# Performance work log

Measured on AMD Instinct MI355X. Metric: run time of the kernel, lower is better.

The kernel has to match this reference:

```python
import jax, jax.numpy as jnp
import numpy as np
from math import sqrt

D, H, B, L = 1024, 16, 2, 2048
DK = D // H

def linear(x, w, b):
    # torch Linear layout: w (out, in)
    return x @ w.T + b

def conv1d(x, w, b, padding, groups=1):
    # x: (B, C, L); w: (O, I/groups, K) -> torch Conv1d semantics
    y = jax.lax.conv_general_dilated(
        x, w, window_strides=(1,), padding=(padding,),
        dimension_numbers=('NCH', 'OIH', 'NCH'), feature_group_count=groups)
    return y + b[None, :, None]

def setup_inputs() -> dict:
    key = jax.random.key(0)
    ks = jax.random.split(key, 26)
    def n(k, shape, s=0.02):
        return jax.random.normal(k, shape, jnp.float32) * s
    return {
        'x': jax.random.normal(ks[0], (B, L, D), jnp.float32),
        'Wq_w': n(ks[1], (D, D)), 'Wq_b': n(ks[2], (D,)),
        'Wk_w': n(ks[3], (D, D)), 'Wk_b': n(ks[4], (D,)),
        'Wv_w': n(ks[5], (D, D)), 'Wv_b': n(ks[6], (D,)),
        'convq_w': n(ks[7], (D, D, 3)), 'convq_b': n(ks[8], (D,)),
        'convk_w': n(ks[9], (D, D, 3)), 'convk_b': n(ks[10], (D,)),
        'qproj_w': n(ks[11], (D, 2 * D)), 'qproj_b': n(ks[12], (D,)),
        'kproj_w': n(ks[13], (D, 2 * D)), 'kproj_b': n(ks[14], (D,)),
        'tau1_w': n(ks[15], (2 * D, 1, 3)), 'tau1_b': n(ks[16], (2 * D,)),
        'tau2_w': n(ks[17], (H, 2 * D, 1)), 'tau2_b': n(ks[18], (H,)),
        'del1_w': n(ks[19], (2 * D, 1, 3)), 'del1_b': n(ks[20], (2 * D,)),
        'del2_w': n(ks[21], (H, 2 * D, 1)), 'del2_b': n(ks[22], (H,)),
        'out_w': n(ks[23], (D, D)), 'out_b': n(ks[24], (D,)),
    }

def reference(x, Wq_w, Wq_b, Wk_w, Wk_b, Wv_w, Wv_b,
              convq_w, convq_b, convk_w, convk_b,
              qproj_w, qproj_b, kproj_w, kproj_b,
              tau1_w, tau1_b, tau2_w, tau2_b,
              del1_w, del1_b, del2_w, del2_b,
              out_w, out_b):
    b_, l_, _ = x.shape

    # Q branch: linear -> conv3 -> concat -> proj
    q_in = linear(x, Wq_w, Wq_b).transpose(0, 2, 1)          # (B, D, L)
    Q3 = conv1d(q_in, convq_w, convq_b, (1, 1))              # (B, D, L)
    Q_cat = jnp.concatenate([q_in, Q3], axis=1).transpose(0, 2, 1)  # (B, L, 2D)
    Q = linear(Q_cat, qproj_w, qproj_b).reshape(b_, l_, H, DK).transpose(0, 2, 1, 3)

    # K branch
    k_in = linear(x, Wk_w, Wk_b).transpose(0, 2, 1)
    K3 = conv1d(k_in, convk_w, convk_b, (1, 1))
    K_cat = jnp.concatenate([k_in, K3], axis=1).transpose(0, 2, 1)
    K = linear(K_cat, kproj_w, kproj_b).reshape(b_, l_, H, DK).transpose(0, 2, 1, 3)

    V = linear(x, Wv_w, Wv_b).reshape(b_, l_, H, DK).transpose(0, 2, 1, 3)

    # per-head tau (query-row scale) and delta (key-column bias), shape (B, H, L)
    x_conv = x.transpose(0, 2, 1)                             # (B, D, L)
    tau = jax.nn.sigmoid(conv1d(
        jax.nn.gelu(conv1d(x_conv, tau1_w, tau1_b, (1, 1), groups=D), approximate=False),
        tau2_w, tau2_b, (0, 0)))
    delta = jax.nn.sigmoid(conv1d(
        jax.nn.gelu(conv1d(x_conv, del1_w, del1_b, (1, 1), groups=D), approximate=False),
        del2_w, del2_b, (0, 0)))

    scores = jnp.einsum('bhqd,bhkd->bhqk', Q, K) / sqrt(DK)   # (B, H, L, L)
    scores = scores * tau[..., None] + delta[:, :, None, :]
    attn = jax.nn.softmax(scores, axis=-1)                    # dropout = identity (eval)
    out = jnp.einsum('bhqk,bhkd->bhqd', attn, V)
    out = out.transpose(0, 2, 1, 3).reshape(b_, l_, D)
    return linear(out, out_w, out_b)
```

## Files before the change

### kernel.cpp

```cpp
#include <hip/hip_runtime.h>

typedef __bf16 bf16_t;
typedef __bf16 bf16x8 __attribute__((ext_vector_type(8)));
typedef __bf16 bf16x4 __attribute__((ext_vector_type(4)));
typedef float f32x4 __attribute__((ext_vector_type(4)));

__device__ __forceinline__ void gload_lds16(const bf16_t* g, bf16_t* l) {
  __builtin_amdgcn_global_load_lds(
      (__attribute__((address_space(1))) void*)g,
      (__attribute__((address_space(3))) void*)l, 16, 0, 0);
}

__global__ void k_detect(const unsigned int* __restrict__ xw, int* __restrict__ flag) {
  __shared__ int red[256];
  int c = 0;
  for (int j = 0; j < 16; ++j) {
    unsigned int w = xw[threadIdx.x + (j << 8)];
    unsigned int e = (w >> 7) & 0xFF;
    c += (e >= 100 && e <= 150) ? 1 : 0;
  }
  red[threadIdx.x] = c;
  __syncthreads();
  for (int s = 128; s > 0; s >>= 1) {
    if (threadIdx.x < s) red[threadIdx.x] += red[threadIdx.x + s];
    __syncthreads();
  }
  if (threadIdx.x == 0) flag[0] = (red[0] > 2048) ? 1 : 0;
}

__device__ __constant__ long c_offs[26] = {
    0, 4194304, 4195328, 4196352, 4197376, 4198400, 4199424, 6296576,
    6297600, 8394752, 8395776, 8401920, 8403968, 8436736, 8436752,
    8442896, 8444944, 8477712, 8477728,
    0, 1048576, 2097152, 3145728,
    0, 1048576, 1049600};
struct CanonArgs { const void* src[18]; };

__global__ void k_canon(CanonArgs a, int base, int n, const int* __restrict__ flag,
                        bf16_t* __restrict__ dst) {
  long e0 = ((long)blockIdx.x * 256 + threadIdx.x) * 8;
  if (e0 >= c_offs[base + n]) return;
  int k = 0;
  while (e0 >= c_offs[base + k + 1]) ++k;
  const long rel = e0 - c_offs[base + k];
  if (flag[0]) {
    *(bf16x8*)&dst[e0] = *(const bf16x8*)((const bf16_t*)a.src[k] + rel);
  } else {
    const float* sf = (const float*)a.src[k] + rel;
    f32x4 lo = *(const f32x4*)sf;
    f32x4 hi = *(const f32x4*)(sf + 4);
    bf16x8 o;
    o[0] = (bf16_t)lo[0]; o[1] = (bf16_t)lo[1]; o[2] = (bf16_t)lo[2]; o[3] = (bf16_t)lo[3];
    o[4] = (bf16_t)hi[0]; o[5] = (bf16_t)hi[1]; o[6] = (bf16_t)hi[2]; o[7] = (bf16_t)hi[3];
    *(bf16x8*)&dst[e0] = o;
  }
}

__global__ void k_zero_pads(bf16_t* __restrict__ pad, bf16_t* __restrict__ zvec) {
  int idx = blockIdx.x * 256 + threadIdx.x;
  if (idx < 1024) zvec[idx] = (bf16_t)0.0f;
  if (idx >= 8192) return;
  int b = idx >> 11;
  int r = (idx >> 10) & 1;
  int c = idx & 1023;
  long row = (long)b * 2050 + (r ? 2049 : 0);
  pad[row * 1024 + c] = (bf16_t)0.0f;
}

__global__ __launch_bounds__(256) void k_ctT(
    const void* __restrict__ wq, const void* __restrict__ wk,
    bf16_t* __restrict__ dq, bf16_t* __restrict__ dk,
    const int* __restrict__ flag) {
  __shared__ bf16_t T[64][72];
  int blk = blockIdx.x;
  const int br = blk >= 768;
  if (br) blk -= 768;
  const void* w = br ? wk : wq;
  bf16_t* dst = br ? dk : dq;
  const int ot = blk / 48, jt = blk - ot * 48;
  const int o0 = ot << 6, j0 = jt << 6;
  const int t = threadIdx.x;
  const int f = flag[0];
#pragma unroll
  for (int it = 0; it < 2; ++it) {
    const int ch = t + (it << 8);
    const int r = ch >> 3, c8 = (ch & 7) << 3;
    const long off = (long)(o0 + r) * 3072 + j0 + c8;
    if (f) {
      *(bf16x8*)&T[r][c8] = *(const bf16x8*)((const bf16_t*)w + off);
    } else {
      const float* sf = (const float*)w + off;
      bf16x8 o8;
#pragma unroll
      for (int e = 0; e < 8; ++e) o8[e] = (bf16_t)sf[e];
      *(bf16x8*)&T[r][c8] = o8;
    }
  }
  __syncthreads();
  const int j = t >> 2, oc0 = (t & 3) << 4;
  const int jj = j0 + j;
  const int drow = (jj % 3) * 1024 + jj / 3;
  bf16_t* dp = dst + (long)drow * 1024 + o0 + oc0;
#pragma unroll
  for (int s = 0; s < 16; ++s) dp[s] = T[oc0 + s][j];
}

__global__ void k_addwp1(bf16_t* __restrict__ Hq, bf16_t* __restrict__ Hk,
                         const bf16_t* __restrict__ qp, const bf16_t* __restrict__ kp) {
  const long e0 = ((long)blockIdx.x * 256 + threadIdx.x) * 8;
  if (e0 >= 2097152L) return;
  const int br = (int)(e0 >> 20);
  const int rem = (int)(e0 & 1048575);
  const int o = rem >> 10, i = rem & 1023;
  bf16_t* h = (br ? Hk : Hq) + (long)o * 3072 + 1024 + i;
  const bf16_t* w = (br ? kp : qp) + (long)o * 2048 + i;
  bf16x8 a = *(const bf16x8*)h;
  bf16x8 b = *(const bf16x8*)w;
  bf16x8 r;
#pragma unroll
  for (int e = 0; e < 8; ++e) r[e] = (bf16_t)((float)a[e] + (float)b[e]);
  *(bf16x8*)h = r;
}

__global__ __launch_bounds__(256) void k_bvec(
    const bf16_t* __restrict__ qp, const bf16_t* __restrict__ kp,
    const bf16_t* __restrict__ cqb, const bf16_t* __restrict__ ckb,
    const bf16_t* __restrict__ qpb, const bf16_t* __restrict__ kpb,
    bf16_t* __restrict__ bvec) {
  const int idx = blockIdx.x * 256 + threadIdx.x;
  if (idx >= 2048) return;
  const int br = idx >> 10, o = idx & 1023;
  const bf16_t* wrow = (br ? kp : qp) + (long)o * 2048 + 1024;
  const bf16_t* cb = br ? ckb : cqb;
  float s = 0.f;
  for (int m8 = 0; m8 < 1024; m8 += 8) {
    bf16x8 w8 = *(const bf16x8*)&wrow[m8];
    bf16x8 c8 = *(const bf16x8*)&cb[m8];
#pragma unroll
    for (int e = 0; e < 8; ++e) s += (float)w8[e] * (float)c8[e];
  }
  bvec[idx] = (bf16_t)(s + (float)((br ? kpb : qpb)[o]));
}

struct GemmP {
  const bf16_t *A0;
  const bf16_t *B0, *B1, *B2;
  const bf16_t *bias0, *bias1, *bias2;
  bf16_t *C0, *C1, *C2;
  long a_jump, at_jump;
  long cj0, cj1, cj2, ct_jump;
  long b_jump;
  int rpb, rpt, lda, ldb, bsel_by_n, bshift, K, csel_by_n;
  int crs0, ccs0, crs1, ccs1, crs2, ccs2;
};

template <int BN, bool FINAL>
__global__ __launch_bounds__(256) void k_gemm(GemmP p, const int* __restrict__ flagp) {
  __shared__ __align__(16) bf16_t As[2][4096];
  __shared__ __align__(16) bf16_t Bs[2][BN * 32];
  const int tid = threadIdx.x;
  const int gx = gridDim.x;
  int lin = blockIdx.y * gx + blockIdx.x;
  const int nwg = gx * gridDim.y;
  lin = ((lin & 7) * (nwg >> 3)) + (lin >> 3);
  const int n0 = (lin % gx) * BN;
  const int m0 = (lin / gx) << 7;
  const int batch = m0 / p.rpb;
  const int tap = (m0 - batch * p.rpb) / p.rpt;
  const int bidx = p.bsel_by_n ? (n0 >> 10) : (m0 >> p.bshift);
  const bf16_t* Bp = p.b_jump ? (p.B0 + (long)bidx * p.b_jump)
                              : (bidx == 0 ? p.B0 : (bidx == 1 ? p.B1 : p.B2));
  const bf16_t* biasp = bidx == 0 ? p.bias0 : (bidx == 1 ? p.bias1 : p.bias2);
  const long abase = (long)batch * p.a_jump + (long)tap * p.at_jump;
  const int arow = tid >> 2;
  const int koff = (((tid & 3) ^ ((tid >> 3) & 3)) << 3);
  const int wid = tid >> 6, lane = tid & 63;
  const int l15 = lane & 15, lg = lane >> 4;
  const int nloc = n0 & 1023;

  constexpr int MI = (BN == 128) ? 4 : 2;
  const int wr = (BN == 128) ? ((wid >> 1) << 6) : (wid << 5);
  const int wc = (BN == 128) ? ((wid & 1) << 6) : 0;
  const int rsw = ((lg ^ (l15 >> 1)) & 3) << 3;

  f32x4 acc[MI][4];
#pragma unroll
  for (int i = 0; i < MI; ++i)
#pragma unroll
    for (int j = 0; j < 4; ++j) acc[i][j] = (f32x4){0.f, 0.f, 0.f, 0.f};

  auto stage = [&](int bufi, int k) {
    const int kg = k + koff;
#pragma unroll
    for (int half = 0; half < 2; ++half) {
      const int row = m0 + half * 64 + arow;
      gload_lds16(p.A0 + abase + (long)row * p.lda + kg,
                  &As[bufi][half * 2048 + (tid << 3)]);
    }
    gload_lds16(Bp + (long)(nloc + arow) * p.ldb + kg, &Bs[bufi][tid << 3]);
    if (BN == 128)
      gload_lds16(Bp + (long)(nloc + 64 + arow) * p.ldb + kg, &Bs[bufi][2048 + (tid << 3)]);
  };

  const int nk = p.K >> 5;
  int buf = 0;
  stage(0, 0);
  asm volatile("s_waitcnt vmcnt(0)" ::: "memory");
  __builtin_amdgcn_s_barrier();
  __builtin_amdgcn_sched_barrier(0);
  for (int kt = 0; kt < nk; ++kt) {
    if (kt + 1 < nk) stage(buf ^ 1, (kt + 1) << 5);
    bf16x8 af[MI], bfr[4];
#pragma unroll
    for (int i = 0; i < MI; ++i)
      af[i] = *(const bf16x8*)&As[buf][((wr + (i << 4) + l15) << 5) + rsw];
#pragma unroll
    for (int j = 0; j < 4; ++j)
      bfr[j] = *(const bf16x8*)&Bs[buf][((wc + (j << 4) + l15) << 5) + rsw];
#pragma unroll
    for (int i = 0; i < MI; ++i)
#pragma unroll
      for (int j = 0; j < 4; ++j)
        acc[i][j] = __builtin_amdgcn_mfma_f32_16x16x32_bf16(af[i], bfr[j], acc[i][j], 0, 0, 0);
    if (kt + 1 < nk) asm volatile("s_waitcnt vmcnt(0)" ::: "memory");
    __builtin_amdgcn_s_barrier();
    __builtin_amdgcn_sched_barrier(0);
    buf ^= 1;
  }

  const int cp = p.csel_by_n ? (n0 >> 10) : (m0 >> p.bshift);
  bf16_t* Cb = cp == 0 ? p.C0 : (cp == 1 ? p.C1 : p.C2);
  const int crs = cp == 0 ? p.crs0 : (cp == 1 ? p.crs1 : p.crs2);
  const int ccs = cp == 0 ? p.ccs0 : (cp == 1 ? p.ccs1 : p.ccs2);
  const long cj = cp == 0 ? p.cj0 : (cp == 1 ? p.cj1 : p.cj2);
  const bool f32out = FINAL && (flagp[0] == 0);
  const long cbase = (long)batch * cj + (long)tap * p.ct_jump;
#pragma unroll
  for (int i = 0; i < MI; ++i) {
    const int row = m0 + wr + (i << 4) + (lg << 2);
#pragma unroll
    for (int j = 0; j < 4; ++j) {
      const int col = nloc + wc + (j << 4) + l15;
      const float bv = (float)biasp[col];
#pragma unroll
      for (int r = 0; r < 4; ++r) {
        const float val = acc[i][j][r] + bv;
        const long ci = cbase + (long)(row + r) * crs + (long)col * ccs;
        if (FINAL && f32out) ((float*)Cb)[ci] = val;
        else Cb[ci] = (bf16_t)val;
      }
    }
  }
}

__global__ __launch_bounds__(256) void k_taudelta(
    const bf16_t* __restrict__ x,
    const bf16_t* __restrict__ t1w, const bf16_t* __restrict__ t1b,
    const bf16_t* __restrict__ t2w, const bf16_t* __restrict__ t2b,
    const bf16_t* __restrict__ d1w, const bf16_t* __restrict__ d1b,
    const bf16_t* __restrict__ d2w, const bf16_t* __restrict__ d2b,
    float* __restrict__ tau, float* __restrict__ dlt)
{
  const int bt = blockIdx.x;
  const int t = bt & 2047;
  const int b = bt >> 11;
  const int tid = threadIdx.x;
  const bf16_t* xr = x + ((long)bt << 10);

  float acc[32];
#pragma unroll
  for (int i = 0; i < 32; ++i) acc[i] = 0.f;

  for (int j = 0; j < 8; ++j) {
    const int c = tid + (j << 8);
    const int src = c >> 1;
    const float x0 = (float)xr[src];
    const float xm = (t > 0) ? (float)xr[src - 1024] : 0.f;
    const float xp = (t < 2047) ? (float)xr[src + 1024] : 0.f;
    float st = (float)t1w[3 * c] * xm + (float)t1w[3 * c + 1] * x0 +
               (float)t1w[3 * c + 2] * xp + (float)t1b[c];
    float sd = (float)d1w[3 * c] * xm + (float)d1w[3 * c + 1] * x0 +
               (float)d1w[3 * c + 2] * xp + (float)d1b[c];
    const float gt = 0.5f * st * (1.f + erff(st * 0.70710678118f));
    const float gd = 0.5f * sd * (1.f + erff(sd * 0.70710678118f));
#pragma unroll
    for (int h = 0; h < 16; ++h) {
      acc[h]      += (float)t2w[(h << 11) + c] * gt;
      acc[16 + h] += (float)d2w[(h << 11) + c] * gd;
    }
  }

  __shared__ float red[256][33];
  __shared__ float red2[8][32];
#pragma unroll
  for (int i = 0; i < 32; ++i) red[tid][i] = acc[i];
  __syncthreads();
  const int i = tid & 31, g = tid >> 5;
  float p = 0.f;
#pragma unroll
  for (int k2 = 0; k2 < 32; ++k2) p += red[(g << 5) + k2][i];
  __syncthreads();
  red2[g][i] = p;
  __syncthreads();
  if (tid < 32) {
    float s = 0.f;
#pragma unroll
    for (int g2 = 0; g2 < 8; ++g2) s += red2[g2][tid];
    const int h = tid & 15;
    if (tid < 16) {
      s += (float)t2b[h];
      tau[((long)((b << 4) + h) << 11) + t] = 1.f / (1.f + __expf(-s));
    } else {
      s += (float)d2b[h];
      dlt[((long)((b << 4) + h) << 11) + t] =
          1.4426950408889634f / (1.f + __expf(-s));
    }
  }
}

__device__ __forceinline__ unsigned pk2(float a, float b) {
  union { bf16_t h[2]; unsigned u; } z;
  z.h[0] = (bf16_t)a; z.h[1] = (bf16_t)b;
  return z.u;
}

__global__ __launch_bounds__(256) void k_attn(
    const bf16_t* __restrict__ QKb, const bf16_t* __restrict__ VT,
    const float* __restrict__ tau, const float* __restrict__ dlt,
    bf16_t* __restrict__ O)
{
  const int lin = blockIdx.x;
  const int wg = ((lin & 7) << 7) + (lin >> 3);
  const int bh = wg >> 5, qt = wg & 31;
  const int tid = threadIdx.x;
  const int lane = tid & 63;
  const int wid = tid >> 6;
  const int l15 = lane & 15, lg = lane >> 4;
  const int b = bh >> 4, h = bh & 15;
  const int qbase = (qt << 6) + (wid << 4);

  const bf16_t* Qp = QKb + ((long)b << 21) + (h << 6);
  const bf16_t* Kp = QKb + 4194304 + ((long)b << 21) + (h << 6);
  const bf16_t* Vp = VT + ((long)bh << 17);
  const float* dltb = dlt + ((long)bh << 11);

  __shared__ __align__(16) bf16_t Ks[2][4096];
  __shared__ __align__(16) bf16_t Vs[2][4096];
  __shared__ unsigned Plds[4][16][32];

  bf16x8 qf[2];
#pragma unroll
  for (int kd = 0; kd < 2; ++kd)
    qf[kd] = *(const bf16x8*)&Qp[((long)(qbase + l15) << 10) + (kd << 5) + (lg << 3)];
  const float tq = tau[((long)bh << 11) + qbase + l15] * (0.125f * 1.4426950408889634f);

  bf16x8 onesf;
#pragma unroll
  for (int e = 0; e < 8; ++e) onesf[e] = (bf16_t)1.0f;

  f32x4 accO[4];
#pragma unroll
  for (int d = 0; d < 4; ++d) accO[d] = (f32x4){0.f, 0.f, 0.f, 0.f};
  f32x4 accL = (f32x4){0.f, 0.f, 0.f, 0.f};

  const int xr = (l15 & 7) << 2;

  auto stageKV = [&](int bufi, int kk) {
#pragma unroll
    for (int it = 0; it < 2; ++it) {
      const int t2 = tid + (it << 8);
      const int r = t2 >> 3, cc = (t2 & 7) ^ (r & 7);
      gload_lds16(Kp + ((long)(kk + r) << 10) + (cc << 3), &Ks[bufi][t2 << 3]);
    }
#pragma unroll
    for (int it = 0; it < 2; ++it) {
      const int t2 = tid + (it << 8);
      const int r = t2 >> 3;
      gload_lds16(Vp + ((long)r << 11) + kk + (((t2 & 7) ^ (r & 7)) << 3), &Vs[bufi][t2 << 3]);
    }
  };

  int buf = 0;
  stageKV(0, 0);
  asm volatile("s_waitcnt vmcnt(0)" ::: "memory");
  __builtin_amdgcn_s_barrier();
  __builtin_amdgcn_sched_barrier(0);

  for (int kk = 0; kk < 2048; kk += 64) {
    if (kk + 64 < 2048) stageKV(buf ^ 1, kk + 64);

    f32x4 st[4];
    __builtin_amdgcn_s_setprio(1);
#pragma unroll
    for (int kb = 0; kb < 4; ++kb) {
      f32x4 z = (f32x4){0.f, 0.f, 0.f, 0.f};
#pragma unroll
      for (int kd = 0; kd < 2; ++kd) {
        const bf16x8 kf = *(const bf16x8*)&Ks[buf][(((kb << 4) + l15) << 6) +
                                                  ((((kd << 2) | lg) ^ (l15 & 7)) << 3)];
        z = __builtin_amdgcn_mfma_f32_16x16x32_bf16(kf, qf[kd], z, 0, 0, 0);
      }
      st[kb] = z;
    }
    __builtin_amdgcn_s_setprio(0);

#pragma unroll
    for (int kb = 0; kb < 4; ++kb) {
      const f32x4 dl = *(const f32x4*)&dltb[kk + (kb << 4) + (lg << 2)];
      const float p0 = exp2f(fminf(fmaf(st[kb][0], tq, dl[0]), 30.f));
      const float p1 = exp2f(fminf(fmaf(st[kb][1], tq, dl[1]), 30.f));
      const float p2 = exp2f(fminf(fmaf(st[kb][2], tq, dl[2]), 30.f));
      const float p3 = exp2f(fminf(fmaf(st[kb][3], tq, dl[3]), 30.f));
      Plds[wid][l15][((kb << 3) + (lg << 1)) ^ xr]       = pk2(p0, p1);
      Plds[wid][l15][(((kb << 3) + (lg << 1)) | 1) ^ xr] = pk2(p2, p3);
    }
    asm volatile("s_waitcnt lgkmcnt(0)" ::: "memory");
    __builtin_amdgcn_sched_barrier(0);
    const bf16x8 pf0 = *(const bf16x8*)&Plds[wid][l15][(lg << 2) ^ xr];
    const bf16x8 pf1 = *(const bf16x8*)&Plds[wid][l15][(16 | (lg << 2)) ^ xr];
    asm volatile("s_waitcnt lgkmcnt(0)" ::: "memory");
    __builtin_amdgcn_sched_barrier(0);

    __builtin_amdgcn_s_setprio(1);
#pragma unroll
    for (int d = 0; d < 4; ++d) {
      const bf16x8 vf0 = *(const bf16x8*)&Vs[buf][(((d << 4) + l15) << 6) +
                                                 ((lg ^ (l15 & 7)) << 3)];
      const bf16x8 vf1 = *(const bf16x8*)&Vs[buf][(((d << 4) + l15) << 6) +
                                                 (((4 | lg) ^ (l15 & 7)) << 3)];
      accO[d] = __builtin_amdgcn_mfma_f32_16x16x32_bf16(vf0, pf0, accO[d], 0, 0, 0);
      accO[d] = __builtin_amdgcn_mfma_f32_16x16x32_bf16(vf1, pf1, accO[d], 0, 0, 0);
    }
    accL = __builtin_amdgcn_mfma_f32_16x16x32_bf16(onesf, pf0, accL, 0, 0, 0);
    accL = __builtin_amdgcn_mfma_f32_16x16x32_bf16(onesf, pf1, accL, 0, 0, 0);
    __builtin_amdgcn_s_setprio(0);

    if (kk + 64 < 2048) asm volatile("s_waitcnt vmcnt(0)" ::: "memory");
    __builtin_amdgcn_s_barrier();
    __builtin_amdgcn_sched_barrier(0);
    buf ^= 1;
  }

  bf16_t* Ob = O + ((long)b << 21) + (h << 6);
  const float inv = 1.f / accL[0];
#pragma unroll
  for (int d = 0; d < 4; ++d) {
    bf16x4 ov;
#pragma unroll
    for (int r = 0; r < 4; ++r) ov[r] = (bf16_t)(accO[d][r] * inv);
    *(bf16x4*)&Ob[((long)(qbase + l15) << 10) + (d << 4) + (lg << 2)] = ov;
  }
}

extern "C" void kernel_launch(void* const* d_in, const int* in_sizes, int n_in,
                              void* d_out, int out_size, void* d_ws, size_t ws_size,
                              hipStream_t stream) {
  char* w = (char*)d_ws;
  int* flag     = (int*)w;
  bf16_t* canon = (bf16_t*)(w + 16);
  bf16_t* pad   = (bf16_t*)(w + 16955472);
  bf16_t* swq   = (bf16_t*)(w + 33749072);
  bf16_t* cvout = (bf16_t*)(w + 40040528);
  bf16_t* QKb   = (bf16_t*)(w + 48429136);
  bf16_t* VT    = (bf16_t*)(w + 65206352);

  bf16_t* xc      = canon;
  bf16_t* Wq_b    = canon + 4194304;
  bf16_t* Wk_b    = canon + 4195328;
  bf16_t* Wv_b    = canon + 4196352;
  bf16_t* convq_b = canon + 4197376;
  bf16_t* convk_b = canon + 4198400;
  bf16_t* qproj_w = canon + 4199424;
  bf16_t* qproj_b = canon + 6296576;
  bf16_t* kproj_w = canon + 6297600;
  bf16_t* kproj_b = canon + 8394752;
  bf16_t* tau1_w  = canon + 8395776;
  bf16_t* tau1_b  = canon + 8401920;
  bf16_t* tau2_w  = canon + 8403968;
  bf16_t* tau2_b  = canon + 8436736;
  bf16_t* del1_w  = canon + 8436752;
  bf16_t* del1_b  = canon + 8442896;
  bf16_t* del2_w  = canon + 8444944;
  bf16_t* del2_b  = canon + 8477712;

  bf16_t* pad_q = pad;
  bf16_t* Wq_w = swq, *Wk_w = swq + 1048576, *Wv_w = swq + 2097152;
  float* tau = (float*)swq;
  float* dlt = (float*)((char*)swq + 262144);
  bf16_t* bvec = (bf16_t*)((char*)swq + 524288);
  bf16_t* zvec = (bf16_t*)((char*)swq + 528384);
  bf16_t* ctT_q = QKb;
  bf16_t* ctT_k = QKb + 3145728;
  bf16_t* Hq = cvout;
  bf16_t* Hk = xc;
  const long hk_delta = (long)(Hk - Hq);
  bf16_t* outw_bf = pad;
  bf16_t* outb_bf = pad + 1048576;
  bf16_t* attn_out = xc;

  k_detect<<<1, 256, 0, stream>>>((const unsigned int*)d_in[0], flag);

  CanonArgs ca{};
  {
    const int idxA[18] = {0, 2, 4, 6, 8, 10, 11, 12, 13, 14,
                          15, 16, 17, 18, 19, 20, 21, 22};
    for (int i = 0; i < 18; ++i) ca.src[i] = d_in[idxA[i]];
    k_canon<<<4140, 256, 0, stream>>>(ca, 0, 18, flag, canon);
  }
  {
    CanonArgs cw{};
    cw.src[0] = d_in[1]; cw.src[1] = d_in[3]; cw.src[2] = d_in[5];
    k_canon<<<1536, 256, 0, stream>>>(cw, 19, 3, flag, swq);
  }
  k_zero_pads<<<32, 256, 0, stream>>>(pad, zvec);

  {
    GemmP p{};
    p.A0 = xc;
    p.B0 = Wq_w; p.B1 = Wk_w; p.B2 = Wv_w;
    p.bias0 = Wq_b; p.bias1 = Wk_b; p.bias2 = Wv_b;
    p.C0 = pad_q + 1024; p.C1 = pad_q + 4198400 + 1024; p.C2 = VT;
    p.a_jump = 0; p.at_jump = 0;
    p.cj0 = 2048; p.cj1 = 2048; p.cj2 = 2095104; p.ct_jump = 0;
    p.b_jump = 0;
    p.rpb = 2048; p.rpt = 1 << 30; p.lda = 1024; p.ldb = 1024;
    p.bsel_by_n = 1; p.bshift = 12; p.K = 1024; p.csel_by_n = 1;
    p.crs0 = 1024; p.ccs0 = 1; p.crs1 = 1024; p.ccs1 = 1; p.crs2 = 1; p.ccs2 = 2048;
    k_gemm<128, false><<<dim3(24, 32), 256, 0, stream>>>(p, flag);
  }

  k_taudelta<<<4096, 256, 0, stream>>>(xc, tau1_w, tau1_b, tau2_w, tau2_b,
                                       del1_w, del1_b, del2_w, del2_b, tau, dlt);

  k_ctT<<<1536, 256, 0, stream>>>(d_in[7], d_in[9], ctT_q, ctT_k, flag);

  {
    GemmP p{};
    p.A0 = qproj_w + 1024;
    p.B0 = ctT_q; p.B1 = ctT_q; p.B2 = ctT_q;
    p.bias0 = p.bias1 = p.bias2 = zvec;
    p.C0 = p.C1 = p.C2 = Hq;
    p.a_jump = (long)(kproj_w - qproj_w) - 3072L * 2048;
    p.at_jump = -2097152;
    p.cj0 = p.cj1 = p.cj2 = hk_delta - 9437184;
    p.ct_jump = -3144704;
    p.b_jump = 1048576;
    p.rpb = 3072; p.rpt = 1024; p.lda = 2048; p.ldb = 1024;
    p.bsel_by_n = 0; p.bshift = 10; p.K = 1024; p.csel_by_n = 0;
    p.crs0 = p.crs1 = p.crs2 = 3072; p.ccs0 = p.ccs1 = p.ccs2 = 1;
    k_gemm<128, false><<<dim3(8, 48), 256, 0, stream>>>(p, flag);
  }

  k_addwp1<<<1024, 256, 0, stream>>>(Hq, Hk, qproj_w, kproj_w);
  k_bvec<<<8, 256, 0, stream>>>(qproj_w, kproj_w, convq_b, convk_b,
                                qproj_b, kproj_b, bvec);

  {
    GemmP p{};
    p.A0 = pad;
    p.B0 = Hq; p.B1 = Hk; p.B2 = Hk;
    p.bias0 = bvec; p.bias1 = bvec + 1024; p.bias2 = bvec + 1024;
    p.C0 = p.C1 = p.C2 = QKb;
    p.a_jump = 4096; p.at_jump = 2048;
    p.cj0 = p.cj1 = p.cj2 = 0; p.ct_jump = 0;
    p.b_jump = 0;
    p.rpb = 4096; p.rpt = 2048; p.lda = 1024; p.ldb = 3072;
    p.bsel_by_n = 0; p.bshift = 12; p.K = 3072; p.csel_by_n = 0;
    p.crs0 = p.crs1 = p.crs2 = 1024; p.ccs0 = p.ccs1 = p.ccs2 = 1;
    k_gemm<128, false><<<dim3(8, 64), 256, 0, stream>>>(p, flag);
  }

  {
    CanonArgs co{};
    co.src[0] = d_in[23]; co.src[1] = d_in[24];
    k_canon<<<513, 256, 0, stream>>>(co, 23, 2, flag, outw_bf);
  }

  k_attn<<<1024, 256, 0, stream>>>(QKb, VT, tau, dlt, attn_out);

  {
    GemmP p{};
    p.A0 = attn_out;
    p.B0 = p.B1 = p.B2 = outw_bf;
    p.bias0 = p.bias1 = p.bias2 = outb_bf;
    p.C0 = p.C1 = p.C2 = (bf16_t*)d_out;
    p.a_jump = 0; p.at_jump = 0;
    p.cj0 = p.cj1 = p.cj2 = 0; p.ct_jump = 0;
    p.b_jump = 0;
    p.rpb = 1 << 30; p.rpt = 1 << 30; p.lda = 1024; p.ldb = 1024;
    p.bsel_by_n = 0; p.bshift = 12; p.K = 1024; p.csel_by_n = 0;
    p.crs0 = p.crs1 = p.crs2 = 1024; p.ccs0 = p.ccs1 = p.ccs2 = 1;
    k_gemm<64, true><<<dim3(16, 32), 256, 0, stream>>>(p, flag);
  }
}
```

Before: 405.4 us.

## Process two 16-row query subtiles per wave in attention kernel

Each wave now handles 32 query rows as two 16-row subtiles, so a workgroup covers 128 queries and the grid is halved to 512 blocks. K and V fragments read from LDS and the staged K/V tiles are reused across both subtiles, which halves K/V global loads and LDS reads per unit of work. The cost is roughly double the accumulator and P registers, which may lower occupancy, plus fewer workgroups to fill the GPU.

```diff
diff --git a/kernel.cpp b/kernel.cpp
--- a/kernel.cpp
+++ b/kernel.cpp
@@ -330,14 +330,14 @@
     bf16_t* __restrict__ O)
 {
   const int lin = blockIdx.x;
-  const int wg = ((lin & 7) << 7) + (lin >> 3);
-  const int bh = wg >> 5, qt = wg & 31;
+  const int wg = ((lin & 7) << 6) + (lin >> 3);
+  const int bh = wg >> 4, qt = wg & 15;
   const int tid = threadIdx.x;
   const int lane = tid & 63;
   const int wid = tid >> 6;
   const int l15 = lane & 15, lg = lane >> 4;
   const int b = bh >> 4, h = bh & 15;
-  const int qbase = (qt << 6) + (wid << 4);
+  const int qb0 = (qt << 7) + (wid << 5);
 
   const bf16_t* Qp = QKb + ((long)b << 21) + (h << 6);
   const bf16_t* Kp = QKb + 4194304 + ((long)b << 21) + (h << 6);
@@ -346,22 +346,30 @@
 
   __shared__ __align__(16) bf16_t Ks[2][4096];
   __shared__ __align__(16) bf16_t Vs[2][4096];
-  __shared__ unsigned Plds[4][16][32];
-
-  bf16x8 qf[2];
-#pragma unroll
-  for (int kd = 0; kd < 2; ++kd)
-    qf[kd] = *(const bf16x8*)&Qp[((long)(qbase + l15) << 10) + (kd << 5) + (lg << 3)];
-  const float tq = tau[((long)bh << 11) + qbase + l15] * (0.125f * 1.4426950408889634f);
+  __shared__ unsigned Plds[4][2][16][32];
+
+  bf16x8 qf[2][2];
+  float tq[2];
+#pragma unroll
+  for (int s = 0; s < 2; ++s) {
+#pragma unroll
+    for (int kd = 0; kd < 2; ++kd)
+      qf[s][kd] = *(const bf16x8*)&Qp[((long)(qb0 + (s << 4) + l15) << 10) + (kd << 5) + (lg << 3)];
+    tq[s] = tau[((long)bh << 11) + qb0 + (s << 4) + l15] * (0.125f * 1.4426950408889634f);
+  }
 
   bf16x8 onesf;
 #pragma unroll
   for (int e = 0; e < 8; ++e) onesf[e] = (bf16_t)1.0f;
 
-  f32x4 accO[4];
-#pragma unroll
-  for (int d = 0; d < 4; ++d) accO[d] = (f32x4){0.f, 0.f, 0.f, 0.f};
-  f32x4 accL = (f32x4){0.f, 0.f, 0.f, 0.f};
+  f32x4 accO[2][4];
+#pragma unroll
+  for (int s = 0; s < 2; ++s)
+#pragma unroll
+    for (int d = 0; d < 4; ++d) accO[s][d] = (f32x4){0.f, 0.f, 0.f, 0.f};
+  f32x4 accL[2];
+  accL[0] = (f32x4){0.f, 0.f, 0.f, 0.f};
+  accL[1] = (f32x4){0.f, 0.f, 0.f, 0.f};
 
   const int xr = (l15 & 7) << 2;
 
@@ -389,35 +397,44 @@
   for (int kk = 0; kk < 2048; kk += 64) {
     if (kk + 64 < 2048) stageKV(buf ^ 1, kk + 64);
 
-    f32x4 st[4];
+    f32x4 st[2][4];
     __builtin_amdgcn_s_setprio(1);
 #pragma unroll
     for (int kb = 0; kb < 4; ++kb) {
-      f32x4 z = (f32x4){0.f, 0.f, 0.f, 0.f};
-#pragma unroll
-      for (int kd = 0; kd < 2; ++kd) {
-        const bf16x8 kf = *(const bf16x8*)&Ks[buf][(((kb << 4) + l15) << 6) +
-                                                  ((((kd << 2) | lg) ^ (l15 & 7)) << 3)];
-        z = __builtin_amdgcn_mfma_f32_16x16x32_bf16(kf, qf[kd], z, 0, 0, 0);
+      const bf16x8 kf0 = *(const bf16x8*)&Ks[buf][(((kb << 4) + l15) << 6) +
+                                                 ((lg ^ (l15 & 7)) << 3)];
+      const bf16x8 kf1 = *(const bf16x8*)&Ks[buf][(((kb << 4) + l15) << 6) +
+                                                 (((4 | lg) ^ (l15 & 7)) << 3)];
+#pragma unroll
+      for (int s = 0; s < 2; ++s) {
+        f32x4 z = (f32x4){0.f, 0.f, 0.f, 0.f};
+        z = __builtin_amdgcn_mfma_f32_16x16x32_bf16(kf0, qf[s][0], z, 0, 0, 0);
+        z = __builtin_amdgcn_mfma_f32_16x16x32_bf16(kf1, qf[s][1], z, 0, 0, 0);
+        st[s][kb] = z;
       }
-      st[kb] = z;
     }
     __builtin_amdgcn_s_setprio(0);
 
 #pragma unroll
-    for (int kb = 0; kb < 4; ++kb) {
-      const f32x4 dl = *(const f32x4*)&dltb[kk + (kb << 4) + (lg << 2)];
-      const float p0 = exp2f(fminf(fmaf(st[kb][0], tq, dl[0]), 30.f));
-      const float p1 = exp2f(fminf(fmaf(st[kb][1], tq, dl[1]), 30.f));
-      const float p2 = exp2f(fminf(fmaf(st[kb][2], tq, dl[2]), 30.f));
-      const float p3 = exp2f(fminf(fmaf(st[kb][3], tq, dl[3]), 30.f));
-      Plds[wid][l15][((kb << 3) + (lg << 1)) ^ xr]       = pk2(p0, p1);
-      Plds[wid][l15][(((kb << 3) + (lg << 1)) | 1) ^ xr] = pk2(p2, p3);
-    }
+    for (int s = 0; s < 2; ++s)
+#pragma unroll
+      for (int kb = 0; kb < 4; ++kb) {
+        const f32x4 dl = *(const f32x4*)&dltb[kk + (kb << 4) + (lg << 2)];
+        const float p0 = exp2f(fminf(fmaf(st[s][kb][0], tq[s], dl[0]), 30.f));
+        const float p1 = exp2f(fminf(fmaf(st[s][kb][1], tq[s], dl[1]), 30.f));
+        const float p2 = exp2f(fminf(fmaf(st[s][kb][2], tq[s], dl[2]), 30.f));
+        const float p3 = exp2f(fminf(fmaf(st[s][kb][3], tq[s], dl[3]), 30.f));
+        Plds[wid][s][l15][((kb << 3) + (lg << 1)) ^ xr]       = pk2(p0, p1);
+        Plds[wid][s][l15][(((kb << 3) + (lg << 1)) | 1) ^ xr] = pk2(p2, p3);
+      }
     asm volatile("s_waitcnt lgkmcnt(0)" ::: "memory");
     __builtin_amdgcn_sched_barrier(0);
-    const bf16x8 pf0 = *(const bf16x8*)&Plds[wid][l15][(lg << 2) ^ xr];
-    const bf16x8 pf1 = *(const bf16x8*)&Plds[wid][l15][(16 | (lg << 2)) ^ xr];
+    bf16x8 pf[2][2];
+#pragma unroll
+    for (int s = 0; s < 2; ++s) {
+      pf[s][0] = *(const bf16x8*)&Plds[wid][s][l15][(lg << 2) ^ xr];
+      pf[s][1] = *(const bf16x8*)&Plds[wid][s][l15][(16 | (lg << 2)) ^ xr];
+    }
     asm volatile("s_waitcnt lgkmcnt(0)" ::: "memory");
     __builtin_amdgcn_sched_barrier(0);
 
@@ -428,11 +445,17 @@
                                                  ((lg ^ (l15 & 7)) << 3)];
       const bf16x8 vf1 = *(const bf16x8*)&Vs[buf][(((d << 4) + l15) << 6) +
                                                  (((4 | lg) ^ (l15 & 7)) << 3)];
-      accO[d] = __builtin_amdgcn_mfma_f32_16x16x32_bf16(vf0, pf0, accO[d], 0, 0, 0);
-      accO[d] = __builtin_amdgcn_mfma_f32_16x16x32_bf16(vf1, pf1, accO[d], 0, 0, 0);
-    }
-    accL = __builtin_amdgcn_mfma_f32_16x16x32_bf16(onesf, pf0, accL, 0, 0, 0);
-    accL = __builtin_amdgcn_mfma_f32_16x16x32_bf16(onesf, pf1, accL, 0, 0, 0);
+#pragma unroll
+      for (int s = 0; s < 2; ++s) {
+        accO[s][d] = __builtin_amdgcn_mfma_f32_16x16x32_bf16(vf0, pf[s][0], accO[s][d], 0, 0, 0);
+        accO[s][d] = __builtin_amdgcn_mfma_f32_16x16x32_bf16(vf1, pf[s][1], accO[s][d], 0, 0, 0);
+      }
+    }
+#pragma unroll
+    for (int s = 0; s < 2; ++s) {
+      accL[s] = __builtin_amdgcn_mfma_f32_16x16x32_bf16(onesf, pf[s][0], accL[s], 0, 0, 0);
+      accL[s] = __builtin_amdgcn_mfma_f32_16x16x32_bf16(onesf, pf[s][1], accL[s], 0, 0, 0);
+    }
     __builtin_amdgcn_s_setprio(0);
 
     if (kk + 64 < 2048) asm volatile("s_waitcnt vmcnt(0)" ::: "memory");
@@ -442,13 +465,16 @@
   }
 
   bf16_t* Ob = O + ((long)b << 21) + (h << 6);
-  const float inv = 1.f / accL[0];
-#pragma unroll
-  for (int d = 0; d < 4; ++d) {
-    bf16x4 ov;
-#pragma unroll
-    for (int r = 0; r < 4; ++r) ov[r] = (bf16_t)(accO[d][r] * inv);
-    *(bf16x4*)&Ob[((long)(qbase + l15) << 10) + (d << 4) + (lg << 2)] = ov;
+#pragma unroll
+  for (int s = 0; s < 2; ++s) {
+    const float inv = 1.f / accL[s][0];
+#pragma unroll
+    for (int d = 0; d < 4; ++d) {
+      bf16x4 ov;
+#pragma unroll
+      for (int r = 0; r < 4; ++r) ov[r] = (bf16_t)(accO[s][d][r] * inv);
+      *(bf16x4*)&Ob[((long)(qb0 + (s << 4) + l15) << 10) + (d << 4) + (lg << 2)] = ov;
+    }
   }
 }
 
@@ -576,7 +602,7 @@
     k_canon<<<513, 256, 0, stream>>>(co, 23, 2, flag, outw_bf);
   }
 
-  k_attn<<<1024, 256, 0, stream>>>(QKb, VT, tau, dlt, attn_out);
+  k_attn<<<512, 256, 0, stream>>>(QKb, VT, tau, dlt, attn_out);
 
   {
     GemmP p{};
```

New measurement: 408.7 us. No clear change (+0.8%).
